# Kernel optimization log

Hardware: AMD Instinct MI355X
Metric: run time of the kernel (lower is better)

The kernel has to match this reference:

```python
import jax, jax.numpy as jnp
import numpy as np

D_MODEL = 256
D_INNER = 512          # expand * d_model
HEADDIM = 64
NHEADS = D_INNER // HEADDIM   # 8
NGROUPS = 1
D_STATE = 64
D_IN_PROJ = 2 * D_INNER + 2 * NGROUPS * D_STATE + NHEADS   # 1160
CONV_DIM = D_INNER + 2 * NGROUPS * D_STATE                  # 640
LN_EPS = 1e-5


def setup_inputs() -> dict:
    key = jax.random.key(0)
    ks = jax.random.split(key, 16)
    s = 0.02
    # dt_bias init as in torch code
    dt = jnp.exp(jax.random.uniform(ks[10], (NHEADS,)) * (np.log(0.1) - np.log(0.001)) + np.log(0.001))
    dt = jnp.clip(dt, 1e-4)
    dt_bias = dt + jnp.log(-jnp.expm1(-dt))
    A_log = jnp.log(jax.random.uniform(ks[11], (NHEADS,), minval=1.0, maxval=16.0))
    return {
        "u": jax.random.normal(ks[0], (4, 8192, D_MODEL), dtype=jnp.float32),
        "H": 64,
        "W": 128,
        "W_in": jax.random.normal(ks[1], (D_IN_PROJ, D_MODEL), dtype=jnp.float32) * s,
        "W_stereo": jax.random.normal(ks[2], (D_IN_PROJ, D_INNER), dtype=jnp.float32) * s,
        "conv_l_w": jax.random.normal(ks[3], (CONV_DIM, 1, 3, 3), dtype=jnp.float32) * 0.1,
        "conv_l_b": jax.random.normal(ks[4], (CONV_DIM,), dtype=jnp.float32) * 0.01,
        "conv_r_w": jax.random.normal(ks[5], (CONV_DIM, 1, 3, 3), dtype=jnp.float32) * 0.1,
        "conv_r_b": jax.random.normal(ks[6], (CONV_DIM,), dtype=jnp.float32) * 0.01,
        "conv_w": jax.random.normal(ks[7], (CONV_DIM, 1, 3, 3), dtype=jnp.float32) * 0.1,
        "conv_b": jax.random.normal(ks[8], (CONV_DIM,), dtype=jnp.float32) * 0.01,
        "dt_bias": dt_bias,
        "A_log": A_log,
        "D_l": jnp.ones((NHEADS,), dtype=jnp.float32),
        "D_r": jnp.ones((NHEADS,), dtype=jnp.float32),
        "D": jnp.ones((NHEADS,), dtype=jnp.float32),
        "ln_g": jnp.ones((D_INNER,), dtype=jnp.float32),
        "ln_b": jnp.zeros((D_INNER,), dtype=jnp.float32),
        "W_out": jax.random.normal(ks[9], (D_MODEL, D_INNER), dtype=jnp.float32) * s,
    }


def _dwconv(x, w, b):
    # x: (B, C, H, W); depthwise 3x3 conv, SAME padding ((d_conv-1)//2 = 1)
    y = jax.lax.conv_general_dilated(
        x, w, window_strides=(1, 1), padding='SAME',
        dimension_numbers=('NCHW', 'OIHW', 'NCHW'),
        feature_group_count=CONV_DIM)
    return y + b[None, :, None, None]


def _layernorm(x, g, b):
    mu = x.mean(-1, keepdims=True)
    var = x.var(-1, keepdims=True)
    return (x - mu) / jnp.sqrt(var + LN_EPS) * g + b


def _lin_attn(x, dt, A, Bm, Cm, Dp):
    # x: (b, l, d_inner), dt: (b, l, h), Bm/Cm: (b, l, d_state); ngroups == 1
    b, l, _ = x.shape
    xh = x.reshape(b, l, NHEADS, HEADDIM)              # V: (b, l, h, p)
    dA = -(dt[..., None] * A[None, None, :, None])     # ssd_positve_dA -> -dt*A, (b,l,h,1)
    KV = jnp.einsum('bls,blhp->bhsp', Bm, xh * dA)     # K^T @ V_scaled
    y = jnp.einsum('bls,bhsp->blhp', Cm, KV)           # Q @ KV
    y = y + xh * Dp[None, None, :, None]               # skip D
    return y.reshape(b, l, D_INNER)


def reference(u, H, W, W_in, W_stereo, conv_l_w, conv_l_b, conv_r_w, conv_r_b,
              conv_w, conv_b, dt_bias, A_log, D_l, D_r, D, ln_g, ln_b, W_out):
    batch, seqlen, _ = u.shape
    half = batch // 2
    silu = jax.nn.silu
    A = -jnp.exp(A_log)

    zxbcdt = u @ W_in.T                                             # (b, l, 1160)
    z, xBC, dt = jnp.split(zxbcdt, [D_INNER, D_INNER + CONV_DIM], axis=-1)
    dt = jax.nn.softplus(dt + dt_bias)                              # (b, l, h)

    xBC = xBC.reshape(batch, H, W, CONV_DIM).transpose(0, 3, 1, 2)  # NCHW
    xBC1 = silu(_dwconv(xBC[:half], conv_l_w, conv_l_b)).transpose(0, 2, 3, 1).reshape(half, H * W, CONV_DIM)
    xBC2 = silu(_dwconv(xBC[half:], conv_r_w, conv_r_b)).transpose(0, 2, 3, 1).reshape(half, H * W, CONV_DIM)

    x1, B1, C1 = jnp.split(xBC1, [D_INNER, D_INNER + NGROUPS * D_STATE], axis=-1)
    x2, B2, C2 = jnp.split(xBC2, [D_INNER, D_INNER + NGROUPS * D_STATE], axis=-1)
    dt1, dt2 = dt[:half], dt[half:]

    y1 = _layernorm(_lin_attn(x1, dt1, A, B1, C1, D_l), ln_g, ln_b)
    y2 = _layernorm(_lin_attn(x2, dt2, A, B2, C2, D_r), ln_g, ln_b)
    y = jnp.concatenate([y1, y2], axis=0) * z

    zxs = y @ W_stereo.T
    zs, xBCs, dts = jnp.split(zxs, [D_INNER, D_INNER + CONV_DIM], axis=-1)
    dts = jax.nn.softplus(dts + dt_bias)

    xBCs = xBCs.reshape(batch, H, W, CONV_DIM).transpose(0, 3, 1, 2)
    xBCs = silu(_dwconv(xBCs, conv_w, conv_b)).transpose(0, 2, 3, 1).reshape(batch, H * W, CONV_DIM)
    xs, Bs, Cs = jnp.split(xBCs, [D_INNER, D_INNER + NGROUPS * D_STATE], axis=-1)

    ys = _layernorm(_lin_attn(xs, dts, A, Bs, Cs, D), ln_g, ln_b) * zs
    return ys @ W_out.T
```

## Files before the change

### kernel.cpp

```cpp
#include <hip/hip_runtime.h>
#include <hip/hip_bf16.h>
#include <math.h>

#define NB    4
#define LSEQ  8192
#define HH    64
#define WW    128
#define DMODEL 256
#define DINNER 512
#define NH    8
#define DSTATE 64
#define DPROJ 1160
#define CONVD 640
#define MROWS (NB*LSEQ)
#define KVCH  32
#define CBLK  80

typedef unsigned short bf16_t;
typedef __attribute__((ext_vector_type(8))) unsigned short ushort8v;
typedef __attribute__((ext_vector_type(8))) short short8v;
typedef __attribute__((ext_vector_type(4))) float f32x4;

static __device__ __forceinline__ float bf2f(bf16_t u) {
    return __uint_as_float(((unsigned)u) << 16);
}
static __device__ __forceinline__ bf16_t f2bf(float f) {
    unsigned u = __float_as_uint(f);
    u += 0x7FFFu + ((u >> 16) & 1u);
    return (bf16_t)(u >> 16);
}

template <typename TC>
__global__ __launch_bounds__(256) void gemm_mfma_bk64(
    const bf16_t* __restrict__ A, int lda,
    const bf16_t* __restrict__ B, int ldb,
    TC* __restrict__ C, int ldc,
    int M, int N, int K)
{
    __shared__ __align__(16) bf16_t As[2][128 * 64];
    __shared__ __align__(16) bf16_t Bs[2][128 * 64];
    const int nwg = gridDim.x * gridDim.y;
    const int wg  = blockIdx.y * gridDim.x + blockIdx.x;
    const int swz = (wg & 7) * (nwg >> 3) + (wg >> 3);
    const int bx  = swz % gridDim.x;
    const int by  = swz / gridDim.x;

    const int tid = threadIdx.x;
    const int m0 = by * 128;
    const int n0 = bx * 128;
    const int wid = tid >> 6;
    const int lane = tid & 63;
    const int wr = (wid >> 1) * 64;
    const int wc = (wid & 1) * 64;
    const int fr = lane & 15;
    const int kq = lane >> 4;

    f32x4 acc[4][4];
    #pragma unroll
    for (int i = 0; i < 4; ++i)
        #pragma unroll
        for (int j = 0; j < 4; ++j) acc[i][j] = (f32x4){0.f, 0.f, 0.f, 0.f};

    const int srow0 = tid >> 3;
    const int sslot = tid & 7;

#define STAGE_BK64(buf, k0)                                                    \
    {                                                                          \
        _Pragma("unroll")                                                      \
        for (int i = 0; i < 4; ++i) {                                          \
            const int row  = srow0 + i * 32;                                   \
            const int chunk = sslot ^ (row & 7);                               \
            const size_t ga = (size_t)(m0 + row) * lda + (k0) + chunk * 8;     \
            const size_t gb = (size_t)(n0 + row) * ldb + (k0) + chunk * 8;     \
            const int ldst = (i * 256 + tid) * 8;                              \
            __builtin_amdgcn_global_load_lds(                                  \
                (const __attribute__((address_space(1))) void*)(A + ga),       \
                (__attribute__((address_space(3))) void*)(&As[buf][ldst]), 16, 0, 0); \
            __builtin_amdgcn_global_load_lds(                                  \
                (const __attribute__((address_space(1))) void*)(B + gb),       \
                (__attribute__((address_space(3))) void*)(&Bs[buf][ldst]), 16, 0, 0); \
        }                                                                      \
    }

    const int nt = K >> 6;
    STAGE_BK64(0, 0);
    __syncthreads();

    int cur = 0;
    for (int t = 0; t < nt; ++t) {
        if (t + 1 < nt) STAGE_BK64(cur ^ 1, (t + 1) * 64);

        short8v a_frag[2][4], b_frag[2][4];
        #pragma unroll
        for (int ks = 0; ks < 2; ++ks) {
            #pragma unroll
            for (int m = 0; m < 4; ++m) {
                const int row = wr + m * 16 + fr;
                const int slot = (ks * 4 + kq) ^ (fr & 7);
                a_frag[ks][m] = *(const short8v*)&As[cur][row * 64 + slot * 8];
            }
            #pragma unroll
            for (int n = 0; n < 4; ++n) {
                const int row = wc + n * 16 + fr;
                const int slot = (ks * 4 + kq) ^ (fr & 7);
                b_frag[ks][n] = *(const short8v*)&Bs[cur][row * 64 + slot * 8];
            }
        }
        #pragma unroll
        for (int ks = 0; ks < 2; ++ks)
            #pragma unroll
            for (int m = 0; m < 4; ++m)
                #pragma unroll
                for (int n = 0; n < 4; ++n)
                    acc[m][n] = __builtin_amdgcn_mfma_f32_16x16x32_bf16(
                        a_frag[ks][m], b_frag[ks][n], acc[m][n], 0, 0, 0);

        __syncthreads();
        cur ^= 1;
    }
#undef STAGE_BK64

    #pragma unroll
    for (int mi = 0; mi < 4; ++mi) {
        #pragma unroll
        for (int ni = 0; ni < 4; ++ni) {
            const int col = n0 + wc + ni * 16 + fr;
            if (col < N) {
                #pragma unroll
                for (int q = 0; q < 4; ++q) {
                    const int row = m0 + wr + mi * 16 + kq * 4 + q;
                    if constexpr (sizeof(TC) == 2)
                        C[(size_t)row * ldc + col] = f2bf(acc[mi][ni][q]);
                    else
                        C[(size_t)row * ldc + col] = acc[mi][ni][q];
                }
            }
        }
    }
}

template <typename TC>
__global__ __launch_bounds__(256) void gemm_mfma_bt(
    const bf16_t* __restrict__ A, int lda, size_t sAb,
    const bf16_t* __restrict__ B, int ldb, size_t sBb,
    TC* __restrict__ C, int ldc, size_t sCb,
    int M, int N, int K)
{
    __shared__ __align__(16) bf16_t As[128 * 32];
    __shared__ __align__(16) bf16_t Bs[128 * 32];
    const bf16_t* Ab = A + blockIdx.z * sAb;
    const bf16_t* Bb = B + blockIdx.z * sBb;
    TC*            Cb = C + blockIdx.z * sCb;
    const int tid = threadIdx.x;
    const int m0 = blockIdx.y * 128;
    const int n0 = blockIdx.x * 128;
    const int wid = tid >> 6;
    const int lane = tid & 63;
    const int wr = (wid >> 1) * 64;
    const int wc = (wid & 1) * 64;
    const int fr = lane & 15;
    const int fk = (lane >> 4) * 8;

    f32x4 acc[4][4];
    #pragma unroll
    for (int i = 0; i < 4; ++i)
        #pragma unroll
        for (int j = 0; j < 4; ++j) acc[i][j] = (f32x4){0.f, 0.f, 0.f, 0.f};

    const int srow = tid >> 2;
    const int scol = (tid & 3) * 8;
    const bf16_t* gA = Ab + (size_t)(m0 + srow) * lda + scol;
    const bf16_t* gB = Bb + (size_t)(n0 + srow) * ldb + scol;
    bf16_t* lA = As + tid * 8;
    bf16_t* lB = Bs + tid * 8;

    for (int k0 = 0; k0 < K; k0 += 32) {
        __builtin_amdgcn_global_load_lds(
            (const __attribute__((address_space(1))) void*)(gA + k0),
            (__attribute__((address_space(3))) void*)lA, 16, 0, 0);
        __builtin_amdgcn_global_load_lds(
            (const __attribute__((address_space(1))) void*)(gA + (size_t)64 * lda + k0),
            (__attribute__((address_space(3))) void*)(lA + 2048), 16, 0, 0);
        __builtin_amdgcn_global_load_lds(
            (const __attribute__((address_space(1))) void*)(gB + k0),
            (__attribute__((address_space(3))) void*)lB, 16, 0, 0);
        __builtin_amdgcn_global_load_lds(
            (const __attribute__((address_space(1))) void*)(gB + (size_t)64 * ldb + k0),
            (__attribute__((address_space(3))) void*)(lB + 2048), 16, 0, 0);
        __syncthreads();

        short8v a_frag[4], b_frag[4];
        #pragma unroll
        for (int m = 0; m < 4; ++m)
            a_frag[m] = *(const short8v*)&As[(wr + m * 16 + fr) * 32 + fk];
        #pragma unroll
        for (int n = 0; n < 4; ++n)
            b_frag[n] = *(const short8v*)&Bs[(wc + n * 16 + fr) * 32 + fk];
        #pragma unroll
        for (int m = 0; m < 4; ++m)
            #pragma unroll
            for (int n = 0; n < 4; ++n)
                acc[m][n] = __builtin_amdgcn_mfma_f32_16x16x32_bf16(
                    a_frag[m], b_frag[n], acc[m][n], 0, 0, 0);
        __syncthreads();
    }

    #pragma unroll
    for (int mi = 0; mi < 4; ++mi) {
        #pragma unroll
        for (int ni = 0; ni < 4; ++ni) {
            const int col = n0 + wc + ni * 16 + fr;
            if (col < N) {
                #pragma unroll
                for (int q = 0; q < 4; ++q) {
                    const int row = m0 + wr + mi * 16 + (lane >> 4) * 4 + q;
                    if constexpr (sizeof(TC) == 2)
                        Cb[(size_t)row * ldc + col] = f2bf(acc[mi][ni][q]);
                    else
                        Cb[(size_t)row * ldc + col] = acc[mi][ni][q];
                }
            }
        }
    }
}

__global__ __launch_bounds__(256) void cvt_bf16_kernel(
    const float* __restrict__ in, bf16_t* __restrict__ out, int n)
{
    const int base = (blockIdx.x * 256 + threadIdx.x) * 4;
    if (base >= n) return;
    float4 v = *(const float4*)&in[base];
    ushort4 o;
    o.x = f2bf(v.x); o.y = f2bf(v.y); o.z = f2bf(v.z); o.w = f2bf(v.w);
    *(ushort4*)&out[base] = o;
}

__global__ __launch_bounds__(256) void wpad_kernel(
    const float* __restrict__ W, bf16_t* __restrict__ Wp,
    int N, int Npad, int K)
{
    const int i = blockIdx.x * 256 + threadIdx.x;
    if (i >= Npad * K) return;
    const int r = i / K, k = i - r * K;
    Wp[i] = (r < N) ? f2bf(W[(size_t)r * K + k]) : (bf16_t)0;
}

__global__ __launch_bounds__(256) void dt_kernel(
    const bf16_t* __restrict__ zx, const float* __restrict__ dt_bias,
    float* __restrict__ dtbuf)
{
    const int idx = blockIdx.x * 256 + threadIdx.x;
    const int h = idx & 7;
    const int row = idx >> 3;
    const float v = bf2f(zx[(size_t)row * DPROJ + (DINNER + CONVD) + h]) + dt_bias[h];
    const float sp = (v > 0.f) ? (v + log1pf(expf(-v))) : log1pf(expf(v));
    dtbuf[idx] = sp;
}

__global__ __launch_bounds__(256) void conv_silu_kernel(
    const bf16_t* __restrict__ zx,
    const float* __restrict__ wA, const float* __restrict__ bA,
    const float* __restrict__ wB, const float* __restrict__ bB,
    bf16_t* __restrict__ out)
{
    const int idx = blockIdx.x * 256 + threadIdx.x;
    const int cb = idx % CBLK;
    const int pc = idx / CBLK;
    const int c0 = cb * 8;
    const int ww = pc & (WW - 1);
    const int h4 = (pc >> 7) & 15;
    const int b  = pc >> 11;
    const int hbase = h4 * 4;
    const float* wp = (b < 2) ? wA : wB;
    const float* bp = (b < 2) ? bA : bB;

    float w[72];
    const float4* wsrc = (const float4*)(wp + c0 * 9);
    #pragma unroll
    for (int i = 0; i < 18; ++i) ((float4*)w)[i] = wsrc[i];

    float acc[4][8];
    {
        float4 bv0 = *(const float4*)(bp + c0);
        float4 bv1 = *(const float4*)(bp + c0 + 4);
        #pragma unroll
        for (int o = 0; o < 4; ++o) {
            acc[o][0] = bv0.x; acc[o][1] = bv0.y; acc[o][2] = bv0.z; acc[o][3] = bv0.w;
            acc[o][4] = bv1.x; acc[o][5] = bv1.y; acc[o][6] = bv1.z; acc[o][7] = bv1.w;
        }
    }

    const bf16_t* base = zx + (size_t)b * LSEQ * DPROJ + DINNER + c0;
    #pragma unroll
    for (int ri = 0; ri < 6; ++ri) {
        const int hi = hbase + ri - 1;
        const bool hok = (unsigned)hi < (unsigned)HH;
        float cur[3][8];
        #pragma unroll
        for (int kj = 0; kj < 3; ++kj) {
            const int wi = ww + kj - 1;
            if (hok && (unsigned)wi < (unsigned)WW) {
                const ushort8v v = *(const ushort8v*)(base + (size_t)(hi * WW + wi) * DPROJ);
                #pragma unroll
                for (int q = 0; q < 8; ++q) cur[kj][q] = bf2f(v[q]);
            } else {
                #pragma unroll
                for (int q = 0; q < 8; ++q) cur[kj][q] = 0.f;
            }
        }
        #pragma unroll
        for (int o = 0; o < 4; ++o) {
            const int ki = ri - o;
            if (ki >= 0 && ki < 3) {
                #pragma unroll
                for (int kj = 0; kj < 3; ++kj)
                    #pragma unroll
                    for (int q = 0; q < 8; ++q)
                        acc[o][q] += cur[kj][q] * w[q * 9 + ki * 3 + kj];
            }
        }
    }

    #pragma unroll
    for (int o = 0; o < 4; ++o) {
        const int t = b * LSEQ + (hbase + o) * WW + ww;
        ushort8v ov;
        #pragma unroll
        for (int q = 0; q < 8; ++q) {
            const float s = acc[o][q] / (1.f + expf(-acc[o][q]));
            ov[q] = f2bf(s);
        }
        *(ushort8v*)(out + (size_t)t * CONVD + c0) = ov;
    }
}

__global__ __launch_bounds__(128) void kv_part_kernel(
    const bf16_t* __restrict__ xconv, const float* __restrict__ dtbuf,
    const float* __restrict__ A_log, float* __restrict__ KVp)
{
    const int h = blockIdx.y, b = blockIdx.z, chunk = blockIdx.x;
    const int tid = threadIdx.x;
    const int w = tid >> 6, lane = tid & 63;
    __shared__ float lds[2 * 4352];
    float* Bt = lds + w * 4352;
    float* Xt = Bt + 2176;
    const float eA = expf(A_log[h]);
    const int s4  = (lane & 15) * 4;
    const int p16 = (lane >> 4) * 16;
    const int r    = lane & 31;
    const int part = lane >> 5;

    float acc[4][16];
    #pragma unroll
    for (int i = 0; i < 4; ++i)
        #pragma unroll
        for (int j = 0; j < 16; ++j) acc[i][j] = 0.f;

    const int l0 = b * LSEQ + chunk * 256;

    for (int t = 0; t < 8; t += 2) {
        const int row = l0 + (t + w) * 32 + r;
        const bf16_t* src = xconv + (size_t)row * CONVD + (part ? h * 64 : DINNER);
        const float scale = part ? dtbuf[row * NH + h] * eA : 1.f;
        float* dst = part ? &Xt[r * 68] : &Bt[r * 68];
        #pragma unroll
        for (int j = 0; j < 8; ++j) {
            ushort8v v = *(const ushort8v*)(src + j * 8);
            f32x4 lo = {bf2f(v[0]) * scale, bf2f(v[1]) * scale,
                        bf2f(v[2]) * scale, bf2f(v[3]) * scale};
            f32x4 hi = {bf2f(v[4]) * scale, bf2f(v[5]) * scale,
                        bf2f(v[6]) * scale, bf2f(v[7]) * scale};
            *(f32x4*)&dst[j * 8]     = lo;
            *(f32x4*)&dst[j * 8 + 4] = hi;
        }
        __syncthreads();
        #pragma unroll 4
        for (int rr = 0; rr < 32; ++rr) {
            const f32x4 bv = *(const f32x4*)&Bt[rr * 68 + s4];
            #pragma unroll
            for (int q = 0; q < 4; ++q) {
                const f32x4 xv = *(const f32x4*)&Xt[rr * 68 + p16 + q * 4];
                #pragma unroll
                for (int si = 0; si < 4; ++si)
                    #pragma unroll
                    for (int k = 0; k < 4; ++k)
                        acc[si][q * 4 + k] += bv[si] * xv[k];
            }
        }
        __syncthreads();
    }

    if (w == 0) {
        #pragma unroll
        for (int si = 0; si < 4; ++si)
            #pragma unroll
            for (int q = 0; q < 4; ++q)
                *(f32x4*)&lds[(s4 + si) * 68 + p16 + q * 4] =
                    (f32x4){acc[si][q*4], acc[si][q*4+1], acc[si][q*4+2], acc[si][q*4+3]};
    }
    __syncthreads();
    if (w == 1) {
        float* dst = KVp + ((size_t)chunk * (NB * NH) + (b * NH + h)) * 4096;
        #pragma unroll
        for (int si = 0; si < 4; ++si)
            #pragma unroll
            for (int q = 0; q < 4; ++q) {
                const f32x4 o = *(const f32x4*)&lds[(s4 + si) * 68 + p16 + q * 4];
                f32x4 v = {acc[si][q*4] + o[0], acc[si][q*4+1] + o[1],
                           acc[si][q*4+2] + o[2], acc[si][q*4+3] + o[3]};
                *(f32x4*)&dst[(s4 + si) * 64 + p16 + q * 4] = v;
            }
    }
}

__global__ __launch_bounds__(256) void kv_reduce_T_kernel(
    const float* __restrict__ KVp, bf16_t* __restrict__ KVT)
{
    const int idx = blockIdx.x * 256 + threadIdx.x;
    float s = 0.f;
    #pragma unroll
    for (int c = 0; c < KVCH; ++c) s += KVp[(size_t)c * 131072 + idx];
    const int bh = idx >> 12;
    const int ss = (idx >> 6) & 63;
    const int p  = idx & 63;
    KVT[((size_t)(bh * 64 + p)) * 64 + ss] = f2bf(s);
}

__global__ __launch_bounds__(256) void ln_gate_kernel(
    const bf16_t* __restrict__ Yattn, const bf16_t* __restrict__ xconv,
    const bf16_t* __restrict__ zx,
    const float* __restrict__ DA, const float* __restrict__ DB,
    const float* __restrict__ ln_g, const float* __restrict__ ln_b,
    bf16_t* __restrict__ ybuf)
{
    const int w = threadIdx.x >> 6, lane = threadIdx.x & 63;
    const int c0 = lane * 8;
    const int h = lane >> 3;
    float g[8], be[8];
    *(float4*)&g[0]  = *(const float4*)&ln_g[c0];
    *(float4*)&g[4]  = *(const float4*)&ln_g[c0 + 4];
    *(float4*)&be[0] = *(const float4*)&ln_b[c0];
    *(float4*)&be[4] = *(const float4*)&ln_b[c0 + 4];
    const int row0 = (blockIdx.x * 4 + w) * 4;

    for (int i = 0; i < 4; ++i) {
        const int row = row0 + i;
        const int b = row >> 13;
        const float Dv = (b < 2) ? DA[h] : DB[h];
        ushort8v yv = *(const ushort8v*)(Yattn + (size_t)row * DINNER + c0);
        ushort8v xv = *(const ushort8v*)(xconv + (size_t)row * CONVD + c0);
        float y[8];
        float s1 = 0.f, s2 = 0.f;
        #pragma unroll
        for (int q = 0; q < 8; ++q) {
            y[q] = bf2f(yv[q]) + bf2f(xv[q]) * Dv;
            s1 += y[q]; s2 += y[q] * y[q];
        }
        #pragma unroll
        for (int off = 32; off > 0; off >>= 1) {
            s1 += __shfl_xor(s1, off, 64);
            s2 += __shfl_xor(s2, off, 64);
        }
        const float mu = s1 * (1.f / 512.f);
        const float var = s2 * (1.f / 512.f) - mu * mu;
        const float rstd = rsqrtf(var + 1e-5f);
        ushort8v zv = *(const ushort8v*)(zx + (size_t)row * DPROJ + c0);
        ushort8v o;
        #pragma unroll
        for (int q = 0; q < 8; ++q)
            o[q] = f2bf(((y[q] - mu) * rstd * g[q] + be[q]) * bf2f(zv[q]));
        *(ushort8v*)(ybuf + (size_t)row * DINNER + c0) = o;
    }
}

extern "C" void kernel_launch(void* const* d_in, const int* in_sizes, int n_in,
                              void* d_out, int out_size, void* d_ws, size_t ws_size,
                              hipStream_t stream)
{
    const float* u        = (const float*)d_in[0];
    const float* W_in     = (const float*)d_in[3];
    const float* W_st     = (const float*)d_in[4];
    const float* conv_l_w = (const float*)d_in[5];
    const float* conv_l_b = (const float*)d_in[6];
    const float* conv_r_w = (const float*)d_in[7];
    const float* conv_r_b = (const float*)d_in[8];
    const float* conv_w   = (const float*)d_in[9];
    const float* conv_b   = (const float*)d_in[10];
    const float* dt_bias  = (const float*)d_in[11];
    const float* A_log    = (const float*)d_in[12];
    const float* D_l      = (const float*)d_in[13];
    const float* D_r      = (const float*)d_in[14];
    const float* Dp       = (const float*)d_in[15];
    const float* ln_g     = (const float*)d_in[16];
    const float* ln_b     = (const float*)d_in[17];
    const float* W_out    = (const float*)d_in[18];
    float* out = (float*)d_out;

    char* ws = (char*)d_ws;
    const size_t ZX_B    = (size_t)MROWS * DPROJ * 2;
    const size_t XCONV_B = (size_t)MROWS * CONVD * 2;
    const size_t YBUF_B  = (size_t)MROWS * DINNER * 2;
    const size_t DT_B    = (size_t)MROWS * NH * 4;
    const size_t KVT_B   = (size_t)NB * DINNER * 64 * 2;
    const size_t UBF_B   = (size_t)MROWS * DMODEL * 2;
    const size_t WIN_B   = (size_t)1280 * DMODEL * 2;
    const size_t WST_B   = (size_t)1280 * DINNER * 2;
    const size_t WOUT_B  = (size_t)256 * DINNER * 2;
    bf16_t* zx    = (bf16_t*)(ws);
    bf16_t* xconv = (bf16_t*)(ws + ZX_B);
    bf16_t* ybuf  = (bf16_t*)(ws + ZX_B + XCONV_B);
    float*  dtbuf = (float*) (ws + ZX_B + XCONV_B + YBUF_B);
    bf16_t* KVT   = (bf16_t*)(ws + ZX_B + XCONV_B + YBUF_B + DT_B);
    bf16_t* ubf   = (bf16_t*)(ws + ZX_B + XCONV_B + YBUF_B + DT_B + KVT_B);
    float*  KVp   = (float*) (ws + ZX_B + XCONV_B + YBUF_B + DT_B + KVT_B);
    bf16_t* WinP  = (bf16_t*)(ws + ZX_B + XCONV_B + YBUF_B + DT_B + KVT_B + UBF_B);
    bf16_t* WstP  = (bf16_t*)(ws + ZX_B + XCONV_B + YBUF_B + DT_B + KVT_B + UBF_B + WIN_B);
    bf16_t* WoutP = (bf16_t*)(ws + ZX_B + XCONV_B + YBUF_B + DT_B + KVT_B + UBF_B + WIN_B + WST_B);
    bf16_t* Yattn = (bf16_t*)(ws + ZX_B + XCONV_B + YBUF_B + DT_B + KVT_B + UBF_B + WIN_B + WST_B + WOUT_B);

    const dim3 gemmGridP(10, MROWS / 128);
    const dim3 gemmGridO(2,  MROWS / 128);
    const dim3 ymmGrid(4, LSEQ / 128, NB);
    const dim3 kvGrid(KVCH, NH, NB);
    const int convGrid = (MROWS / 4) * CBLK / 256;
    const int lnGrid = MROWS / 16;

    cvt_bf16_kernel<<<(MROWS * DMODEL / 4 + 255) / 256, 256, 0, stream>>>(u, ubf, MROWS * DMODEL);
    wpad_kernel<<<(1280 * DMODEL + 255) / 256, 256, 0, stream>>>(W_in, WinP, DPROJ, 1280, DMODEL);
    wpad_kernel<<<(1280 * DINNER + 255) / 256, 256, 0, stream>>>(W_st, WstP, DPROJ, 1280, DINNER);
    wpad_kernel<<<(256 * DINNER + 255) / 256, 256, 0, stream>>>(W_out, WoutP, DMODEL, 256, DINNER);

    gemm_mfma_bk64<bf16_t><<<gemmGridP, 256, 0, stream>>>(
        ubf, DMODEL, WinP, DMODEL, zx, DPROJ, MROWS, DPROJ, DMODEL);
    dt_kernel<<<(MROWS * NH) / 256, 256, 0, stream>>>(zx, dt_bias, dtbuf);
    conv_silu_kernel<<<convGrid, 256, 0, stream>>>(
        zx, conv_l_w, conv_l_b, conv_r_w, conv_r_b, xconv);
    kv_part_kernel<<<kvGrid, 128, 0, stream>>>(xconv, dtbuf, A_log, KVp);
    kv_reduce_T_kernel<<<131072 / 256, 256, 0, stream>>>(KVp, KVT);
    gemm_mfma_bt<bf16_t><<<ymmGrid, 256, 0, stream>>>(
        xconv + DINNER + DSTATE, CONVD, (size_t)LSEQ * CONVD,
        KVT, 64, (size_t)DINNER * 64,
        Yattn, DINNER, (size_t)LSEQ * DINNER, LSEQ, DINNER, 64);
    ln_gate_kernel<<<lnGrid, 256, 0, stream>>>(
        Yattn, xconv, zx, D_l, D_r, ln_g, ln_b, ybuf);

    gemm_mfma_bk64<bf16_t><<<gemmGridP, 256, 0, stream>>>(
        ybuf, DINNER, WstP, DINNER, zx, DPROJ, MROWS, DPROJ, DINNER);
    dt_kernel<<<(MROWS * NH) / 256, 256, 0, stream>>>(zx, dt_bias, dtbuf);
    conv_silu_kernel<<<convGrid, 256, 0, stream>>>(
        zx, conv_w, conv_b, conv_w, conv_b, xconv);
    kv_part_kernel<<<kvGrid, 128, 0, stream>>>(xconv, dtbuf, A_log, KVp);
    kv_reduce_T_kernel<<<131072 / 256, 256, 0, stream>>>(KVp, KVT);
    gemm_mfma_bt<bf16_t><<<ymmGrid, 256, 0, stream>>>(
        xconv + DINNER + DSTATE, CONVD, (size_t)LSEQ * CONVD,
        KVT, 64, (size_t)DINNER * 64,
        Yattn, DINNER, (size_t)LSEQ * DINNER, LSEQ, DINNER, 64);
    ln_gate_kernel<<<lnGrid, 256, 0, stream>>>(
        Yattn, xconv, zx, Dp, Dp, ln_g, ln_b, ybuf);

    gemm_mfma_bk64<float><<<gemmGridO, 256, 0, stream>>>(
        ybuf, DINNER, WoutP, DINNER, out, DMODEL, MROWS, DMODEL, DINNER);
}
```

Before: 382.3 us.

## Switch projection GEMMs to triple-buffered BK32 pipeline with vmcnt waits

Measured after the change: 387.5 us. About the same (+1.4%).

```diff
diff --git a/kernel.cpp b/kernel.cpp
--- a/kernel.cpp
+++ b/kernel.cpp
@@ -31,14 +31,14 @@
 }
 
 template <typename TC>
-__global__ __launch_bounds__(256) void gemm_mfma_bk64(
+__global__ __launch_bounds__(256) void gemm_mfma_pipe(
     const bf16_t* __restrict__ A, int lda,
     const bf16_t* __restrict__ B, int ldb,
     TC* __restrict__ C, int ldc,
     int M, int N, int K)
 {
-    __shared__ __align__(16) bf16_t As[2][128 * 64];
-    __shared__ __align__(16) bf16_t Bs[2][128 * 64];
+    __shared__ __align__(16) bf16_t As[3][128 * 32];
+    __shared__ __align__(16) bf16_t Bs[3][128 * 32];
     const int nwg = gridDim.x * gridDim.y;
     const int wg  = blockIdx.y * gridDim.x + blockIdx.x;
     const int swz = (wg & 7) * (nwg >> 3) + (wg >> 3);
@@ -61,15 +61,15 @@
         #pragma unroll
         for (int j = 0; j < 4; ++j) acc[i][j] = (f32x4){0.f, 0.f, 0.f, 0.f};
 
-    const int srow0 = tid >> 3;
-    const int sslot = tid & 7;
-
-#define STAGE_BK64(buf, k0)                                                    \
+    const int srow0 = tid >> 2;
+    const int sslot = tid & 3;
+
+#define STAGE_P(buf, k0)                                                       \
     {                                                                          \
         _Pragma("unroll")                                                      \
-        for (int i = 0; i < 4; ++i) {                                          \
-            const int row  = srow0 + i * 32;                                   \
-            const int chunk = sslot ^ (row & 7);                               \
+        for (int i = 0; i < 2; ++i) {                                          \
+            const int row  = srow0 + i * 64;                                   \
+            const int chunk = sslot ^ (row & 3);                               \
             const size_t ga = (size_t)(m0 + row) * lda + (k0) + chunk * 8;     \
             const size_t gb = (size_t)(n0 + row) * ldb + (k0) + chunk * 8;     \
             const int ldst = (i * 256 + tid) * 8;                              \
@@ -82,43 +82,40 @@
         }                                                                      \
     }
 
-    const int nt = K >> 6;
-    STAGE_BK64(0, 0);
-    __syncthreads();
-
-    int cur = 0;
+    const int nt = K >> 5;
+    STAGE_P(0, 0);
+    STAGE_P(1, 32);
+
     for (int t = 0; t < nt; ++t) {
-        if (t + 1 < nt) STAGE_BK64(cur ^ 1, (t + 1) * 64);
-
-        short8v a_frag[2][4], b_frag[2][4];
-        #pragma unroll
-        for (int ks = 0; ks < 2; ++ks) {
+        const int cur = t % 3;
+        if (t + 1 < nt) asm volatile("s_waitcnt vmcnt(4)" ::: "memory");
+        else            asm volatile("s_waitcnt vmcnt(0)" ::: "memory");
+        __builtin_amdgcn_s_barrier();
+        __builtin_amdgcn_sched_barrier(0);
+
+        if (t + 2 < nt) STAGE_P((t + 2) % 3, (t + 2) * 32);
+
+        short8v a_frag[4], b_frag[4];
+        #pragma unroll
+        for (int m = 0; m < 4; ++m) {
+            const int row = wr + m * 16 + fr;
+            const int slot = kq ^ (fr & 3);
+            a_frag[m] = *(const short8v*)&As[cur][row * 32 + slot * 8];
+        }
+        #pragma unroll
+        for (int n = 0; n < 4; ++n) {
+            const int row = wc + n * 16 + fr;
+            const int slot = kq ^ (fr & 3);
+            b_frag[n] = *(const short8v*)&Bs[cur][row * 32 + slot * 8];
+        }
+        #pragma unroll
+        for (int m = 0; m < 4; ++m)
             #pragma unroll
-            for (int m = 0; m < 4; ++m) {
-                const int row = wr + m * 16 + fr;
-                const int slot = (ks * 4 + kq) ^ (fr & 7);
-                a_frag[ks][m] = *(const short8v*)&As[cur][row * 64 + slot * 8];
-            }
-            #pragma unroll
-            for (int n = 0; n < 4; ++n) {
-                const int row = wc + n * 16 + fr;
-                const int slot = (ks * 4 + kq) ^ (fr & 7);
-                b_frag[ks][n] = *(const short8v*)&Bs[cur][row * 64 + slot * 8];
-            }
-        }
-        #pragma unroll
-        for (int ks = 0; ks < 2; ++ks)
-            #pragma unroll
-            for (int m = 0; m < 4; ++m)
-                #pragma unroll
-                for (int n = 0; n < 4; ++n)
-                    acc[m][n] = __builtin_amdgcn_mfma_f32_16x16x32_bf16(
-                        a_frag[ks][m], b_frag[ks][n], acc[m][n], 0, 0, 0);
-
-        __syncthreads();
-        cur ^= 1;
-    }
-#undef STAGE_BK64
+            for (int n = 0; n < 4; ++n)
+                acc[m][n] = __builtin_amdgcn_mfma_f32_16x16x32_bf16(
+                    a_frag[m], b_frag[n], acc[m][n], 0, 0, 0);
+    }
+#undef STAGE_P
 
     #pragma unroll
     for (int mi = 0; mi < 4; ++mi) {
@@ -530,7 +527,7 @@
     wpad_kernel<<<(1280 * DINNER + 255) / 256, 256, 0, stream>>>(W_st, WstP, DPROJ, 1280, DINNER);
     wpad_kernel<<<(256 * DINNER + 255) / 256, 256, 0, stream>>>(W_out, WoutP, DMODEL, 256, DINNER);
 
-    gemm_mfma_bk64<bf16_t><<<gemmGridP, 256, 0, stream>>>(
+    gemm_mfma_pipe<bf16_t><<<gemmGridP, 256, 0, stream>>>(
         ubf, DMODEL, WinP, DMODEL, zx, DPROJ, MROWS, DPROJ, DMODEL);
     dt_kernel<<<(MROWS * NH) / 256, 256, 0, stream>>>(zx, dt_bias, dtbuf);
     conv_silu_kernel<<<convGrid, 256, 0, stream>>>(
@@ -544,7 +541,7 @@
     ln_gate_kernel<<<lnGrid, 256, 0, stream>>>(
         Yattn, xconv, zx, D_l, D_r, ln_g, ln_b, ybuf);
 
-    gemm_mfma_bk64<bf16_t><<<gemmGridP, 256, 0, stream>>>(
+    gemm_mfma_pipe<bf16_t><<<gemmGridP, 256, 0, stream>>>(
         ybuf, DINNER, WstP, DINNER, zx, DPROJ, MROWS, DPROJ, DINNER);
     dt_kernel<<<(MROWS * NH) / 256, 256, 0, stream>>>(zx, dt_bias, dtbuf);
     conv_silu_kernel<<<convGrid, 256, 0, stream>>>(
@@ -558,6 +555,6 @@
     ln_gate_kernel<<<lnGrid, 256, 0, stream>>>(
         Yattn, xconv, zx, Dp, Dp, ln_g, ln_b, ybuf);
 
-    gemm_mfma_bk64<float><<<gemmGridO, 256, 0, stream>>>(
+    gemm_mfma_pipe<float><<<gemmGridO, 256, 0, stream>>>(
         ybuf, DINNER, WoutP, DINNER, out, DMODEL, MROWS, DMODEL, DINNER);
 }
```
